# Kernel tuning notes

Hardware: AMD Instinct MI355X
Metric: run time of the kernel (lower is better)

## Reference

```python
import jax, jax.numpy as jnp
import numpy as np

B = 32; H = 56; W = 56; C = 384; NH = 12; WS = 14; SS = 7
L = H * W; N = WS * WS; HD = C // NH; SCALE = HD ** -0.5; HID = 4 * C
NW = (H // WS) * (W // WS)
EPS = 1e-5

def _relative_index():
    ch = np.arange(WS)[:, None].repeat(WS, 1)
    cw = np.arange(WS)[None, :].repeat(WS, 0)
    coords = np.stack([ch, cw], -1).reshape(-1, 2)  # [N,2]
    rel = coords[:, None, :] - coords[None, :, :]
    rel = rel + (WS - 1)
    rel[:, :, 0] *= 2 * WS - 1
    return rel.sum(-1)  # [N,N], values in [0,(2WS-1)^2)

def _attn_mask():
    img = np.zeros((H, W))
    sl = (slice(0, -WS), slice(-WS, -SS), slice(-SS, None))
    cnt = 0
    for hs in sl:
        for ws_ in sl:
            img[hs, ws_] = cnt; cnt += 1
    mw = img.reshape(H // WS, WS, W // WS, WS).transpose(0, 2, 1, 3).reshape(-1, N)
    am = mw[:, None, :] - mw[:, :, None]  # [nW,N,N]
    return np.where(am != 0, -100.0, 0.0).astype(np.float32)

REL_IDX = jnp.asarray(_relative_index())
MASK = jnp.asarray(_attn_mask())  # [NW,N,N]

def _ln(x, w, b):
    m = jnp.mean(x, -1, keepdims=True)
    v = jnp.mean((x - m) ** 2, -1, keepdims=True)
    return (x - m) * jax.lax.rsqrt(v + EPS) * w + b

def setup_inputs() -> dict:
    key = jax.random.key(0)
    ks = jax.random.split(key, 8)
    s = 0.02
    return {
        "x": jax.random.normal(ks[0], (B, L, C), jnp.float32),
        "norm1_w": jnp.ones((C,), jnp.float32),
        "norm1_b": jnp.zeros((C,), jnp.float32),
        "qkv_w": jax.random.normal(ks[1], (3 * C, C), jnp.float32) * s,
        "qkv_b": jnp.zeros((3 * C,), jnp.float32),
        "proj_w": jax.random.normal(ks[2], (C, C), jnp.float32) * s,
        "proj_b": jnp.zeros((C,), jnp.float32),
        "relative_table": jax.random.normal(ks[3], ((2 * WS - 1) ** 2, 2 * NH), jnp.float32) * s,
        "norm2_w": jnp.ones((C,), jnp.float32),
        "norm2_b": jnp.zeros((C,), jnp.float32),
        "fc1_w": jax.random.normal(ks[4], (HID, C), jnp.float32) * s,
        "fc1_b": jnp.zeros((HID,), jnp.float32),
        "fc2_w": jax.random.normal(ks[5], (C, HID), jnp.float32) * s,
        "fc2_b": jnp.zeros((C,), jnp.float32),
    }

def reference(x, norm1_w, norm1_b, qkv_w, qkv_b, proj_w, proj_b,
              relative_table, norm2_w, norm2_b, fc1_w, fc1_b, fc2_w, fc2_b):
    shortcut = x
    xn = _ln(x, norm1_w, norm1_b).reshape(B, H, W, C)
    # cyclic shift + window partition -> [B*NW, N, C]
    xs = jnp.roll(xn, (-SS, -SS), (1, 2))
    xw = xs.reshape(B, H // WS, WS, W // WS, WS, C).transpose(0, 1, 3, 2, 4, 5).reshape(-1, N, C)
    B_ = B * NW
    qkv = (xw @ qkv_w.T + qkv_b).reshape(B_, N, 3, NH, HD).transpose(2, 0, 3, 1, 4)
    q, k, v = qkv[0] * SCALE, qkv[1], qkv[2]  # [B_,NH,N,HD]
    attn = jnp.einsum('bhnd,bhmd->bhnm', q, k)  # [B_,NH,N,N]
    rel = relative_table[REL_IDX]  # [N,N,2*NH]
    rel = rel.transpose(2, 0, 1)  # [2*NH,N,N]
    bias, rscale = rel[:NH], rel[NH:]
    attn = attn + bias[None]
    attn = attn.reshape(B, NW, NH, N, N) + MASK[None, :, None]
    attn = jax.nn.softmax(attn.reshape(B_, NH, N, N), axis=-1)
    attn = attn * rscale[None]  # multiplicative relative scale AFTER softmax
    out = jnp.einsum('bhnm,bhmd->bhnd', attn, v)
    out = out.transpose(0, 2, 1, 3).reshape(B_, N, C)
    out = out @ proj_w.T + proj_b
    # window reverse + reverse shift
    xr = out.reshape(B, H // WS, W // WS, WS, WS, C).transpose(0, 1, 3, 2, 4, 5).reshape(B, H, W, C)
    xr = jnp.roll(xr, (SS, SS), (1, 2)).reshape(B, L, C)
    x = shortcut + xr
    h = _ln(x, norm2_w, norm2_b)
    h = jax.nn.gelu(h @ fc1_w.T + fc1_b, approximate=False) @ fc2_w.T + fc2_b
    return x + h
```

## Files before the change

### kernel.cpp

```cpp
#include <hip/hip_runtime.h>
#include <hip/hip_bf16.h>
#include <math.h>

#define BDIM 32
#define HDIM 56
#define WDIM 56
#define CDIM 384
#define NHEAD 12
#define WSZ 14
#define SSZ 7
#define LDIM (HDIM*WDIM)
#define NTOK (WSZ*WSZ)
#define HDHEAD (CDIM/NHEAD)
#define HIDDIM (4*CDIM)
#define NWIN 16
#define BWIN (BDIM*NWIN)
#define MROWS (BDIM*LDIM)
#define EPSLN 1e-5f
#define ATTSCALE 0.17677669529663687f

#define KROW 40
#define VROW 232
#define PROW 232

typedef __hip_bfloat16 bf16;
typedef __attribute__((ext_vector_type(8))) short bf16x8;
typedef __attribute__((ext_vector_type(4))) short s16x4;
typedef __attribute__((ext_vector_type(4))) float f32x4;

#define ASYNC16(gp, lp) __builtin_amdgcn_global_load_lds( \
    (__attribute__((address_space(1))) void*)(gp),        \
    (__attribute__((address_space(3))) void*)(lp), 16, 0, 0)

static __device__ __forceinline__ short f2bfs(float x) {
  union { bf16 h; short s; } u; u.h = __float2bfloat16(x); return u.s;
}
static __device__ __forceinline__ float bfs2f(short s) {
  unsigned int u = ((unsigned int)(unsigned short)s) << 16;
  float f; __builtin_memcpy(&f, &u, 4); return f;
}
static __device__ __forceinline__ float tof(float x) { return x; }
static __device__ __forceinline__ float tof(bf16 x)  { return __bfloat162float(x); }

__global__ __launch_bounds__(256) void k_cvt(const float* __restrict__ in,
                                             bf16* __restrict__ out, int n)
{
  int i = blockIdx.x * 256 + threadIdx.x;
  if (i < n) out[i] = __float2bfloat16(in[i]);
}

template<bool WIN, typename TIN>
__global__ __launch_bounds__(128) void k_ln(const TIN* __restrict__ xin,
    const float* __restrict__ gw, const float* __restrict__ gb,
    bf16* __restrict__ out)
{
  int r = blockIdx.x;
  int t = threadIdx.x;
  const TIN* xp = xin + (size_t)r * CDIM;
  float v0 = tof(xp[t]), v1 = tof(xp[t+128]), v2 = tof(xp[t+256]);
  float s  = v0+v1+v2;
  float ss = v0*v0 + v1*v1 + v2*v2;
  #pragma unroll
  for (int o = 32; o > 0; o >>= 1) { s += __shfl_down(s, o); ss += __shfl_down(ss, o); }
  __shared__ float red[4];
  if ((t & 63) == 0) { red[(t>>6)*2] = s; red[(t>>6)*2+1] = ss; }
  __syncthreads();
  float mean = (red[0]+red[2]) * (1.0f/CDIM);
  float var  = (red[1]+red[3]) * (1.0f/CDIM) - mean*mean;
  float rstd = rsqrtf(var + EPSLN);

  size_t orow;
  if (WIN) {
    int b = r / LDIM, l = r % LDIM;
    int h = l / WDIM, w = l % WDIM;
    int h2 = (h + HDIM - SSZ) % HDIM, w2 = (w + WDIM - SSZ) % WDIM;
    int wh = h2 / WSZ, ii = h2 % WSZ, ww = w2 / WSZ, jj = w2 % WSZ;
    int b_ = b*NWIN + wh*4 + ww;
    int n  = ii*WSZ + jj;
    orow = ((size_t)b_*NTOK + n) * CDIM;
  } else {
    orow = (size_t)r * CDIM;
  }
  out[orow+t]     = __float2bfloat16((v0-mean)*rstd*gw[t]     + gb[t]);
  out[orow+t+128] = __float2bfloat16((v1-mean)*rstd*gw[t+128] + gb[t+128]);
  out[orow+t+256] = __float2bfloat16((v2-mean)*rstd*gw[t+256] + gb[t+256]);
}

template<int KD, int EPI>
__global__ __launch_bounds__(256) void k_mgemm(
    const bf16* __restrict__ A, const bf16* __restrict__ Wb,
    const float* __restrict__ bias, const float* __restrict__ aux,
    const bf16* __restrict__ auxb,
    float* __restrict__ outf, bf16* __restrict__ outb, int gx)
{
  __shared__ short As[2][128*64];
  __shared__ short Bs[2][128*64];
  int tid  = threadIdx.x;
  int lane = tid & 63, wid = tid >> 6;
  int c15 = lane & 15, h4 = lane >> 4;
  int wr = wid >> 1, wc = wid & 1;

  int nwg = gridDim.x, bid = blockIdx.x;
  int swz = (bid & 7) * (nwg >> 3) + (bid >> 3);
  int ty = swz / gx, tx = swz - ty * gx;
  int row0 = ty * 128, col0 = tx * 128;

  f32x4 acc[4][4] = {};

  int srow = lane >> 3;
  int skk  = ((lane & 7) ^ srow) * 8;

  const int NT = KD / 64;

  #pragma unroll
  for (int s = 0; s < 4; s++) {
    int c = wid*4 + s;
    ASYNC16(A  + (size_t)(row0 + c*8 + srow)*KD + skk, &As[0][c*512]);
    ASYNC16(Wb + (size_t)(col0 + c*8 + srow)*KD + skk, &Bs[0][c*512]);
  }
  __syncthreads();

  for (int t = 0; t < NT; t++) {
    int cur = t & 1;
    if (t + 1 < NT) {
      int k1 = (t+1)*64;
      #pragma unroll
      for (int s = 0; s < 4; s++) {
        int c = wid*4 + s;
        ASYNC16(A  + (size_t)(row0 + c*8 + srow)*KD + k1 + skk, &As[cur^1][c*512]);
        ASYNC16(Wb + (size_t)(col0 + c*8 + srow)*KD + k1 + skk, &Bs[cur^1][c*512]);
      }
    }
    #pragma unroll
    for (int half = 0; half < 2; half++) {
      bf16x8 af[4], bfr[4];
      int blk8 = ((half << 2) + h4) ^ (c15 & 7);
      #pragma unroll
      for (int m = 0; m < 4; m++) {
        int rr = wr*64 + m*16 + c15;
        af[m] = *reinterpret_cast<const bf16x8*>(&As[cur][rr*64 + blk8*8]);
      }
      #pragma unroll
      for (int n = 0; n < 4; n++) {
        int rr = wc*64 + n*16 + c15;
        bfr[n] = *reinterpret_cast<const bf16x8*>(&Bs[cur][rr*64 + blk8*8]);
      }
      #pragma unroll
      for (int n = 0; n < 4; n++)
        #pragma unroll
        for (int m = 0; m < 4; m++)
          acc[n][m] = __builtin_amdgcn_mfma_f32_16x16x32_bf16(bfr[n], af[m], acc[n][m], 0, 0, 0);
    }
    __syncthreads();
  }

  int rb = row0 + wr*64 + c15;
  int cb = col0 + wc*64 + h4*4;
  #pragma unroll
  for (int m = 0; m < 4; m++) {
    int r = rb + m*16;
    if constexpr (EPI == 0) {
      int b_ = r / NTOK, nn = r % NTOK;
      const size_t QKVSTRIDE = (size_t)BWIN*NHEAD*NTOK*HDHEAD;
      #pragma unroll
      for (int n = 0; n < 4; n++) {
        int c0 = cb + n*16;
        f32x4 v = acc[n][m];
        f32x4 b4 = *(const f32x4*)&bias[c0];
        int which = c0 / CDIM, rem = c0 - which*CDIM;
        int hh = rem >> 5, dd = rem & 31;
        float scl = (which == 0) ? ATTSCALE : 1.f;
        s16x4 o;
        #pragma unroll
        for (int i = 0; i < 4; i++) o[i] = f2bfs((v[i] + b4[i]) * scl);
        *(s16x4*)&outb[(size_t)which*QKVSTRIDE + (((size_t)b_*NHEAD+hh)*NTOK+nn)*HDHEAD + dd] = o;
      }
    } else if constexpr (EPI == 1) {
      int b_ = r / NTOK, nn = r % NTOK;
      int b = b_ >> 4, wi = b_ & 15, wh = wi >> 2, ww = wi & 3;
      int ii = nn / WSZ, jj = nn % WSZ;
      int hh = (wh*WSZ + ii + SSZ) % HDIM;
      int wcc = (ww*WSZ + jj + SSZ) % WDIM;
      size_t rr = ((size_t)b*LDIM + hh*WDIM + wcc) * CDIM;
      #pragma unroll
      for (int n = 0; n < 4; n++) {
        int c0 = cb + n*16;
        f32x4 v = acc[n][m];
        f32x4 b4 = *(const f32x4*)&bias[c0];
        f32x4 a4 = *(const f32x4*)&aux[rr + c0];
        s16x4 o;
        #pragma unroll
        for (int i = 0; i < 4; i++) o[i] = f2bfs(a4[i] + v[i] + b4[i]);
        *(s16x4*)&outb[rr + c0] = o;
      }
    } else if constexpr (EPI == 2) {
      #pragma unroll
      for (int n = 0; n < 4; n++) {
        int c0 = cb + n*16;
        f32x4 v = acc[n][m];
        f32x4 b4 = *(const f32x4*)&bias[c0];
        s16x4 o;
        #pragma unroll
        for (int i = 0; i < 4; i++) {
          float val = v[i] + b4[i];
          val = 0.5f * val * (1.0f + erff(val * 0.70710678118654752f));
          o[i] = f2bfs(val);
        }
        *(s16x4*)&outb[(size_t)r*HIDDIM + c0] = o;
      }
    } else {
      #pragma unroll
      for (int n = 0; n < 4; n++) {
        int c0 = cb + n*16;
        f32x4 v = acc[n][m];
        f32x4 b4 = *(const f32x4*)&bias[c0];
        s16x4 ab = *(const s16x4*)&auxb[(size_t)r*CDIM + c0];
        f32x4 o;
        #pragma unroll
        for (int i = 0; i < 4; i++) o[i] = v[i] + b4[i] + bfs2f(ab[i]);
        *(f32x4*)&outf[(size_t)r*CDIM + c0] = o;
      }
    }
  }
}

__global__ __launch_bounds__(256) void k_attn_mfma(const bf16* __restrict__ q,
    const bf16* __restrict__ k, const bf16* __restrict__ v,
    const float* __restrict__ rt, bf16* __restrict__ out)
{
  __shared__ short  Ks[208*KROW];
  __shared__ short  Vt[32*VROW];
  __shared__ short  Ps[4][16*PROW];
  __shared__ float2 tab2[729];
  __shared__ int    regv[208];

  int blk = blockIdx.x;
  int b_ = blk / NHEAD, head = blk % NHEAD;
  int tid = threadIdx.x, lane = tid & 63, wid = tid >> 6;
  int c15 = lane & 15, h4 = lane >> 4;

  const bf16* kp = k + (size_t)blk*NTOK*HDHEAD;
  const bf16* vp = v + (size_t)blk*NTOK*HDHEAD;
  for (int c = tid; c < 784; c += 256) {
    int m = c >> 2, k8 = (c & 3) * 8;
    *(bf16x8*)&Ks[m*KROW + k8] = *(const bf16x8*)(kp + m*32 + k8);
    bf16x8 vv = *(const bf16x8*)(vp + m*32 + k8);
    #pragma unroll
    for (int j = 0; j < 8; j++) Vt[(k8+j)*VROW + m] = vv[j];
  }
  for (int e = tid; e < 12*KROW; e += 256) Ks[196*KROW + e] = 0;
  for (int e = tid; e < 32*28; e += 256) Vt[(e/28)*VROW + 196 + (e%28)] = 0;
  for (int e = tid; e < 729; e += 256)
    tab2[e] = make_float2(rt[e*2*NHEAD + head], rt[e*2*NHEAD + NHEAD + head]);
  {
    int wi = b_ & 15, wh = wi >> 2, ww = wi & 3;
    for (int e = tid; e < 208; e += 256) {
      int rv = 0;
      if (e < NTOK) {
        int i = e / WSZ, j = e % WSZ;
        int ha = wh*WSZ + i, wa = ww*WSZ + j;
        int rh = ha < (HDIM-WSZ) ? 0 : (ha < (HDIM-SSZ) ? 1 : 2);
        int rw = wa < (WDIM-WSZ) ? 0 : (wa < (WDIM-SSZ) ? 1 : 2);
        rv = rh*3 + rw;
      }
      regv[e] = rv;
    }
  }
  __syncthreads();

  int   moff[13], mreg[13];
  float mpad[13];
  #pragma unroll
  for (int t = 0; t < 13; t++) {
    int m  = t*16 + c15;
    int mm = min(m, NTOK-1);
    moff[t] = (mm/WSZ)*27 + (mm%WSZ);
    mreg[t] = regv[mm];
    mpad[t] = (m >= NTOK) ? -1e30f : 0.f;
  }

  short* myP = &Ps[wid][0];
  #pragma unroll
  for (int i = 0; i < 4; i++) myP[(h4*4+i)*PROW + 208 + c15] = 0;

  bf16* op = out + (size_t)b_*NTOK*CDIM + head*HDHEAD;

  for (int t4 = 0; t4 < 4; t4++) {
    int s = t4*4 + wid;
    if (s < 13) {
      int qrow = min(s*16 + c15, NTOK-1);
      bf16x8 qf = *(const bf16x8*)(q + ((size_t)blk*NTOK + qrow)*HDHEAD + h4*8);

      f32x4 sc[13];
      #pragma unroll
      for (int t = 0; t < 13; t++) {
        bf16x8 kf = *(const bf16x8*)&Ks[(t*16 + c15)*KROW + h4*8];
        sc[t] = __builtin_amdgcn_mfma_f32_16x16x32_bf16(qf, kf, (f32x4){0.f,0.f,0.f,0.f}, 0, 0, 0);
      }

      #pragma unroll
      for (int i = 0; i < 4; i++) {
        int n  = s*16 + h4*4 + i;
        int nc = min(n, NTOK-1);
        int nbase = ((nc/WSZ) + 13)*27 + (nc%WSZ) + 13;
        int nreg  = regv[nc];
        float rr[13];
        float sum = 0.f;
        #pragma unroll
        for (int t = 0; t < 13; t++) {
          float2 hr = tab2[nbase - moff[t]];
          float sv = sc[t][i] + hr.x + ((mreg[t] != nreg) ? -100.f : 0.f) + mpad[t];
          float e = __expf(sv);
          rr[t] = hr.y;
          sc[t][i] = e; sum += e;
        }
        #pragma unroll
        for (int o = 1; o < 16; o <<= 1) sum += __shfl_xor(sum, o);
        float inv = 1.f / sum;
        int prow = h4*4 + i;
        #pragma unroll
        for (int t = 0; t < 13; t++)
          myP[prow*PROW + t*16 + c15] = f2bfs(sc[t][i] * inv * rr[t]);
      }
    }

    __syncthreads();

    if (s < 13) {
      f32x4 o0 = {0.f,0.f,0.f,0.f}, o1 = {0.f,0.f,0.f,0.f};
      #pragma unroll
      for (int t7 = 0; t7 < 7; t7++) {
        bf16x8 pf = *(const bf16x8*)&myP[c15*PROW + t7*32 + h4*8];
        bf16x8 v0 = *(const bf16x8*)&Vt[c15*VROW + t7*32 + h4*8];
        bf16x8 v1 = *(const bf16x8*)&Vt[(16 + c15)*VROW + t7*32 + h4*8];
        o0 = __builtin_amdgcn_mfma_f32_16x16x32_bf16(pf, v0, o0, 0, 0, 0);
        o1 = __builtin_amdgcn_mfma_f32_16x16x32_bf16(pf, v1, o1, 0, 0, 0);
      }

      #pragma unroll
      for (int i = 0; i < 4; i++) {
        int n = s*16 + h4*4 + i;
        if (n < NTOK) {
          op[(size_t)n*CDIM + c15]      = __float2bfloat16(o0[i]);
          op[(size_t)n*CDIM + 16 + c15] = __float2bfloat16(o1[i]);
        }
      }
    }

    __syncthreads();
  }
}

extern "C" void kernel_launch(void* const* d_in, const int* in_sizes, int n_in,
                              void* d_out, int out_size, void* d_ws, size_t ws_size,
                              hipStream_t stream)
{
  const float* x      = (const float*)d_in[0];
  const float* n1w    = (const float*)d_in[1];
  const float* n1b    = (const float*)d_in[2];
  const float* qkv_w  = (const float*)d_in[3];
  const float* qkv_b  = (const float*)d_in[4];
  const float* proj_w = (const float*)d_in[5];
  const float* proj_b = (const float*)d_in[6];
  const float* rt     = (const float*)d_in[7];
  const float* n2w    = (const float*)d_in[8];
  const float* n2b    = (const float*)d_in[9];
  const float* fc1_w  = (const float*)d_in[10];
  const float* fc1_b  = (const float*)d_in[11];
  const float* fc2_w  = (const float*)d_in[12];
  const float* fc2_b  = (const float*)d_in[13];

  char* ws = (char*)d_ws;
  const size_t SZ_BF = (size_t)MROWS * CDIM * 2;
  bf16*  xw      = (bf16*)ws;
  bf16*  attnout = (bf16*)ws;
  bf16*  qkv     = (bf16*)(ws + SZ_BF);
  bf16*  x2b     = (bf16*)(ws + SZ_BF);
  bf16*  hln     = (bf16*)(ws + 2*SZ_BF);
  bf16*  hid     = (bf16*)(ws + 4*SZ_BF);
  const int NQKVW = 3*CDIM*CDIM;
  const int NPROJW = CDIM*CDIM;
  const int NFCW  = HIDDIM*CDIM;
  bf16* wq  = (bf16*)(ws + 4*SZ_BF);
  bf16* wp  = wq + NQKVW;
  bf16* wf1 = (bf16*)ws;
  bf16* wf2 = wf1 + NFCW;
  const size_t QKVSTRIDE = (size_t)BWIN*NHEAD*NTOK*HDHEAD;

  k_cvt<<<(NQKVW+255)/256, 256, 0, stream>>>(qkv_w, wq, NQKVW);
  k_cvt<<<(NPROJW+255)/256, 256, 0, stream>>>(proj_w, wp, NPROJW);

  k_ln<true, float><<<MROWS, 128, 0, stream>>>(x, n1w, n1b, xw);
  k_mgemm<CDIM, 0><<<9*(MROWS/128), 256, 0, stream>>>(
      xw, wq, qkv_b, nullptr, nullptr, nullptr, qkv, 9);
  k_attn_mfma<<<BWIN*NHEAD, 256, 0, stream>>>(
      qkv, qkv + QKVSTRIDE, qkv + 2*QKVSTRIDE, rt, attnout);
  k_mgemm<CDIM, 1><<<3*(MROWS/128), 256, 0, stream>>>(
      attnout, wp, proj_b, x, nullptr, nullptr, x2b, 3);

  k_cvt<<<(NFCW+255)/256, 256, 0, stream>>>(fc1_w, wf1, NFCW);
  k_cvt<<<(NFCW+255)/256, 256, 0, stream>>>(fc2_w, wf2, NFCW);

  k_ln<false, bf16><<<MROWS, 128, 0, stream>>>(x2b, n2w, n2b, hln);
  k_mgemm<CDIM, 2><<<12*(MROWS/128), 256, 0, stream>>>(
      hln, wf1, fc1_b, nullptr, nullptr, nullptr, hid, 12);
  k_mgemm<HIDDIM, 3><<<3*(MROWS/128), 256, 0, stream>>>(
      hid, wf2, fc2_b, nullptr, x2b, (float*)d_out, nullptr, 3);
}
```

Before: 1.116 ms.

## Use 256x128 GEMM tiles with 512 threads and a row-major QKV layout

The GEMM kernel now computes 256x128 output tiles with 8 waves and a single LDS buffer, dropping the double-buffered prefetch in favour of higher per-block reuse of B tiles and reliance on occupancy to hide load latency. The QKV GEMM epilogue now writes a plain row-major [rows, 3C] layout instead of scattering into per-head q/k/v tensors. The attention kernel reads q/k/v with a row stride from that layout. Writes become contiguous, but attention loads turn into strided 64-byte chunks, and the loss of prefetch overlap risks exposing global-load latency.

```diff
diff --git a/kernel.cpp b/kernel.cpp
--- a/kernel.cpp
+++ b/kernel.cpp
@@ -18,6 +18,7 @@
 #define MROWS (BDIM*LDIM)
 #define EPSLN 1e-5f
 #define ATTSCALE 0.17677669529663687f
+#define QKVC (3*CDIM)
 
 #define KROW 40
 #define VROW 232
@@ -87,14 +88,14 @@
 }
 
 template<int KD, int EPI>
-__global__ __launch_bounds__(256) void k_mgemm(
+__global__ __launch_bounds__(512, 4) void k_mgemm(
     const bf16* __restrict__ A, const bf16* __restrict__ Wb,
     const float* __restrict__ bias, const float* __restrict__ aux,
     const bf16* __restrict__ auxb,
     float* __restrict__ outf, bf16* __restrict__ outb, int gx)
 {
-  __shared__ short As[2][128*64];
-  __shared__ short Bs[2][128*64];
+  __shared__ short As[256*64];
+  __shared__ short Bs[128*64];
   int tid  = threadIdx.x;
   int lane = tid & 63, wid = tid >> 6;
   int c15 = lane & 15, h4 = lane >> 4;
@@ -103,7 +104,7 @@
   int nwg = gridDim.x, bid = blockIdx.x;
   int swz = (bid & 7) * (nwg >> 3) + (bid >> 3);
   int ty = swz / gx, tx = swz - ty * gx;
-  int row0 = ty * 128, col0 = tx * 128;
+  int row0 = ty * 256, col0 = tx * 128;
 
   f32x4 acc[4][4] = {};
 
@@ -112,25 +113,20 @@
 
   const int NT = KD / 64;
 
-  #pragma unroll
-  for (int s = 0; s < 4; s++) {
-    int c = wid*4 + s;
-    ASYNC16(A  + (size_t)(row0 + c*8 + srow)*KD + skk, &As[0][c*512]);
-    ASYNC16(Wb + (size_t)(col0 + c*8 + srow)*KD + skk, &Bs[0][c*512]);
-  }
-  __syncthreads();
-
   for (int t = 0; t < NT; t++) {
-    int cur = t & 1;
-    if (t + 1 < NT) {
-      int k1 = (t+1)*64;
-      #pragma unroll
-      for (int s = 0; s < 4; s++) {
-        int c = wid*4 + s;
-        ASYNC16(A  + (size_t)(row0 + c*8 + srow)*KD + k1 + skk, &As[cur^1][c*512]);
-        ASYNC16(Wb + (size_t)(col0 + c*8 + srow)*KD + k1 + skk, &Bs[cur^1][c*512]);
-      }
-    }
+    int k0 = t * 64;
+    #pragma unroll
+    for (int s = 0; s < 4; s++) {
+      int c = wid*4 + s;
+      ASYNC16(A + (size_t)(row0 + c*8 + srow)*KD + k0 + skk, &As[c*512]);
+    }
+    #pragma unroll
+    for (int s = 0; s < 2; s++) {
+      int c = wid*2 + s;
+      ASYNC16(Wb + (size_t)(col0 + c*8 + srow)*KD + k0 + skk, &Bs[c*512]);
+    }
+    __syncthreads();
+
     #pragma unroll
     for (int half = 0; half < 2; half++) {
       bf16x8 af[4], bfr[4];
@@ -138,12 +134,12 @@
       #pragma unroll
       for (int m = 0; m < 4; m++) {
         int rr = wr*64 + m*16 + c15;
-        af[m] = *reinterpret_cast<const bf16x8*>(&As[cur][rr*64 + blk8*8]);
+        af[m] = *reinterpret_cast<const bf16x8*>(&As[rr*64 + blk8*8]);
       }
       #pragma unroll
       for (int n = 0; n < 4; n++) {
         int rr = wc*64 + n*16 + c15;
-        bfr[n] = *reinterpret_cast<const bf16x8*>(&Bs[cur][rr*64 + blk8*8]);
+        bfr[n] = *reinterpret_cast<const bf16x8*>(&Bs[rr*64 + blk8*8]);
       }
       #pragma unroll
       for (int n = 0; n < 4; n++)
@@ -160,20 +156,16 @@
   for (int m = 0; m < 4; m++) {
     int r = rb + m*16;
     if constexpr (EPI == 0) {
-      int b_ = r / NTOK, nn = r % NTOK;
-      const size_t QKVSTRIDE = (size_t)BWIN*NHEAD*NTOK*HDHEAD;
       #pragma unroll
       for (int n = 0; n < 4; n++) {
         int c0 = cb + n*16;
         f32x4 v = acc[n][m];
         f32x4 b4 = *(const f32x4*)&bias[c0];
-        int which = c0 / CDIM, rem = c0 - which*CDIM;
-        int hh = rem >> 5, dd = rem & 31;
-        float scl = (which == 0) ? ATTSCALE : 1.f;
+        float scl = (c0 < CDIM) ? ATTSCALE : 1.f;
         s16x4 o;
         #pragma unroll
         for (int i = 0; i < 4; i++) o[i] = f2bfs((v[i] + b4[i]) * scl);
-        *(s16x4*)&outb[(size_t)which*QKVSTRIDE + (((size_t)b_*NHEAD+hh)*NTOK+nn)*HDHEAD + dd] = o;
+        *(s16x4*)&outb[(size_t)r*QKVC + c0] = o;
       }
     } else if constexpr (EPI == 1) {
       int b_ = r / NTOK, nn = r % NTOK;
@@ -224,8 +216,7 @@
   }
 }
 
-__global__ __launch_bounds__(256) void k_attn_mfma(const bf16* __restrict__ q,
-    const bf16* __restrict__ k, const bf16* __restrict__ v,
+__global__ __launch_bounds__(256) void k_attn_mfma(const bf16* __restrict__ qkv,
     const float* __restrict__ rt, bf16* __restrict__ out)
 {
   __shared__ short  Ks[208*KROW];
@@ -239,12 +230,13 @@
   int tid = threadIdx.x, lane = tid & 63, wid = tid >> 6;
   int c15 = lane & 15, h4 = lane >> 4;
 
-  const bf16* kp = k + (size_t)blk*NTOK*HDHEAD;
-  const bf16* vp = v + (size_t)blk*NTOK*HDHEAD;
+  const bf16* rowbase = qkv + (size_t)b_*NTOK*QKVC + head*HDHEAD;
+  const bf16* kp = rowbase + CDIM;
+  const bf16* vp = rowbase + 2*CDIM;
   for (int c = tid; c < 784; c += 256) {
     int m = c >> 2, k8 = (c & 3) * 8;
-    *(bf16x8*)&Ks[m*KROW + k8] = *(const bf16x8*)(kp + m*32 + k8);
-    bf16x8 vv = *(const bf16x8*)(vp + m*32 + k8);
+    *(bf16x8*)&Ks[m*KROW + k8] = *(const bf16x8*)(kp + (size_t)m*QKVC + k8);
+    bf16x8 vv = *(const bf16x8*)(vp + (size_t)m*QKVC + k8);
     #pragma unroll
     for (int j = 0; j < 8; j++) Vt[(k8+j)*VROW + m] = vv[j];
   }
@@ -289,7 +281,7 @@
     int s = t4*4 + wid;
     if (s < 13) {
       int qrow = min(s*16 + c15, NTOK-1);
-      bf16x8 qf = *(const bf16x8*)(q + ((size_t)blk*NTOK + qrow)*HDHEAD + h4*8);
+      bf16x8 qf = *(const bf16x8*)(rowbase + (size_t)qrow*QKVC + h4*8);
 
       f32x4 sc[13];
       #pragma unroll
@@ -385,25 +377,23 @@
   bf16* wp  = wq + NQKVW;
   bf16* wf1 = (bf16*)ws;
   bf16* wf2 = wf1 + NFCW;
-  const size_t QKVSTRIDE = (size_t)BWIN*NHEAD*NTOK*HDHEAD;
 
   k_cvt<<<(NQKVW+255)/256, 256, 0, stream>>>(qkv_w, wq, NQKVW);
   k_cvt<<<(NPROJW+255)/256, 256, 0, stream>>>(proj_w, wp, NPROJW);
 
   k_ln<true, float><<<MROWS, 128, 0, stream>>>(x, n1w, n1b, xw);
-  k_mgemm<CDIM, 0><<<9*(MROWS/128), 256, 0, stream>>>(
+  k_mgemm<CDIM, 0><<<(MROWS/256)*9, 512, 0, stream>>>(
       xw, wq, qkv_b, nullptr, nullptr, nullptr, qkv, 9);
-  k_attn_mfma<<<BWIN*NHEAD, 256, 0, stream>>>(
-      qkv, qkv + QKVSTRIDE, qkv + 2*QKVSTRIDE, rt, attnout);
-  k_mgemm<CDIM, 1><<<3*(MROWS/128), 256, 0, stream>>>(
+  k_attn_mfma<<<BWIN*NHEAD, 256, 0, stream>>>(qkv, rt, attnout);
+  k_mgemm<CDIM, 1><<<(MROWS/256)*3, 512, 0, stream>>>(
       attnout, wp, proj_b, x, nullptr, nullptr, x2b, 3);
 
   k_cvt<<<(NFCW+255)/256, 256, 0, stream>>>(fc1_w, wf1, NFCW);
   k_cvt<<<(NFCW+255)/256, 256, 0, stream>>>(fc2_w, wf2, NFCW);
 
   k_ln<false, bf16><<<MROWS, 128, 0, stream>>>(x2b, n2w, n2b, hln);
-  k_mgemm<CDIM, 2><<<12*(MROWS/128), 256, 0, stream>>>(
+  k_mgemm<CDIM, 2><<<(MROWS/256)*12, 512, 0, stream>>>(
       hln, wf1, fc1_b, nullptr, nullptr, nullptr, hid, 12);
-  k_mgemm<HIDDIM, 3><<<3*(MROWS/128), 256, 0, stream>>>(
+  k_mgemm<HIDDIM, 3><<<(MROWS/256)*3, 512, 0, stream>>>(
       hid, wf2, fc2_b, nullptr, x2b, (float*)d_out, nullptr, 3);
 }
```

After: 1.043 ms. -6.5%, faster.
